# Kernel optimization log

Measured on AMD Instinct MI355X. Metric: run time of the kernel, lower is better.

Reference implementation:

```python
import jax, jax.numpy as jnp
import numpy as np

N, NFEAT, K, HK = 500000, 64, 8, 64

def _trunc_normal(key, shape, std):
    # torch.nn.init.trunc_normal_ truncates at +/-2 (then scaled by std)
    return jnp.clip(jax.random.normal(key, shape), -2.0, 2.0) * std

def setup_inputs() -> dict:
    key = jax.random.key(0)
    kx, kz, kt = jax.random.split(key, 3)
    x = jax.random.normal(kx, (N, NFEAT), dtype=jnp.float32)
    # stacked ParameterList: z[i] in R^{h_K x n}, t[i] in R^{h_K}
    z = _trunc_normal(kz, (K, HK, NFEAT), 1.0).astype(jnp.float32)  # b_z = 1.0
    t = _trunc_normal(kt, (K, HK), 1.0).astype(jnp.float32)         # b_t = 1.0
    return {"x": x, "z": z, "t": t}

def reference(x, z, t):
    w = jnp.exp(z)                                  # [K, HK, n], positive weights
    g = jnp.einsum('ni,khi->nkh', x, w) + t         # [N, K, HK]
    max_vals = jnp.max(g, axis=2)                   # [N, K] maxout per group
    max_idx = jnp.argmax(g, axis=2)                 # [N, K]
    y = jnp.min(max_vals, axis=1)                   # [N]   min over groups
    min_idx = jnp.argmin(max_vals, axis=1)          # [N]
    # A[min_idx[n], max_idx[n, min_idx[n]]] += 1  (vectorized scatter-add)
    cols = jnp.take_along_axis(max_idx, min_idx[:, None], axis=1)[:, 0]  # [N]
    A = jnp.zeros((K, HK), dtype=jnp.float32).at[min_idx, cols].add(1.0)
    return y, A
```

## Files before the change

### kernel.cpp

```cpp
#include <hip/hip_runtime.h>
#include <math.h>

constexpr int NS    = 500000;
constexpr int NF    = 64;
constexpr int KG    = 8;
constexpr int HKC   = 64;
constexpr int NCELL = KG * HKC;
constexpr int RPW   = 32;
constexpr int TPB   = 1024;
constexpr int NBLK  = 256;
constexpr int NTILE = NS / RPW;
constexpr int NWAVES = NBLK * (TPB / 64);

typedef __attribute__((ext_vector_type(8))) _Float16 half8;
typedef __attribute__((ext_vector_type(4))) float f32x4;

__device__ __forceinline__ float swz16_f(float v) {
    return __int_as_float(__builtin_amdgcn_ds_swizzle(__float_as_int(v), 0x401F));
}
__device__ __forceinline__ int swz16_i(int v) {
    return __builtin_amdgcn_ds_swizzle(v, 0x401F);
}

__global__ void prep_kernel(const float* __restrict__ z,
                            _Float16* __restrict__ w_hi,
                            _Float16* __restrict__ w_lo,
                            float* __restrict__ A) {
    int i = blockIdx.x * blockDim.x + threadIdx.x;
    if (i < KG * HKC * NF) {
        float w = expf(z[i]);
        _Float16 h = (_Float16)w;
        w_hi[i] = h;
        w_lo[i] = (_Float16)(w - (float)h);
    }
    if (i < NCELL) A[i] = 0.0f;
}

__global__ __launch_bounds__(TPB, 4) void monn_mfma_kernel(
    const float* __restrict__ x,
    const _Float16* __restrict__ w_hi,
    const _Float16* __restrict__ w_lo,
    const float* __restrict__ t,
    float* __restrict__ y,
    float* __restrict__ A) {

    __shared__ __align__(16) char smem[2 * KG * 8192];
    __shared__ __align__(16) float t_lds[KG * HKC];
    __shared__ unsigned lhist[NCELL];

    const int tid = threadIdx.x;

    {
        const float4* sh = reinterpret_cast<const float4*>(w_hi);
        const float4* sl = reinterpret_cast<const float4*>(w_lo);
#pragma unroll
        for (int i = 0; i < 4; ++i) {
            const int ci  = i * 1024 + tid;
            const int row = (ci >> 3) & 63;
            const int ch  = ci & 7;
            const int addr = (ci >> 9) * 8192 + row * 128 + ((ch ^ (row & 7)) << 4);
            *reinterpret_cast<float4*>(smem + addr)         = sh[ci];
            *reinterpret_cast<float4*>(smem + 65536 + addr) = sl[ci];
        }
        if (tid < 128)
            reinterpret_cast<float4*>(t_lds)[tid] =
                reinterpret_cast<const float4*>(t)[tid];
        if (tid < NCELL) lhist[tid] = 0u;
    }
    __syncthreads();

    const int lane = tid & 63;
    const int m  = lane & 15;
    const int q  = lane >> 4;
    const int q4 = q * 4;
    const int a32 = ((lane ^ 32) << 2);
    const int x7  = m & 7;
    const int rb0 = m * 128 + (((0 + q) ^ x7) << 4);
    const int rb1 = m * 128 + (((4 + q) ^ x7) << 4);
    const int gwave = blockIdx.x * (TPB / 64) + (tid >> 6);

#pragma unroll 1
    for (int tile = gwave; tile < NTILE; tile += NWAVES) {
        const long base = (long)tile * RPW;

        half8 Xh[2][2], Xl[2][2];
#pragma unroll
        for (int rt = 0; rt < 2; ++rt) {
            const float* xp = x + (base + rt * 16 + m) * NF;
#pragma unroll
            for (int s = 0; s < 2; ++s) {
                const int k0 = s * 32 + q * 8;
                const float4 v0 = *reinterpret_cast<const float4*>(xp + k0);
                const float4 v1 = *reinterpret_cast<const float4*>(xp + k0 + 4);
                const float f[8] = {v0.x, v0.y, v0.z, v0.w, v1.x, v1.y, v1.z, v1.w};
#pragma unroll
                for (int j = 0; j < 8; ++j) {
                    _Float16 h = (_Float16)f[j];
                    Xh[rt][s][j] = h;
                    Xl[rt][s][j] = (_Float16)(f[j] - (float)h);
                }
            }
        }

        float ymin[2] = {INFINITY, INFINITY};
        int   code[2] = {0, 0};

#pragma unroll 2
        for (int g = 0; g < KG; ++g) {
            f32x4 acc[4][2];
#pragma unroll
            for (int c = 0; c < 4; ++c) {
                const float4 tv = *reinterpret_cast<const float4*>(
                    t_lds + g * HKC + c * 16 + q4);
                acc[c][0] = (f32x4){tv.x, tv.y, tv.z, tv.w};
                acc[c][1] = acc[c][0];
            }

#pragma unroll
            for (int s = 0; s < 2; ++s) {
                const int rb = (s ? rb1 : rb0) + g * 8192;
#pragma unroll
                for (int c = 0; c < 4; ++c) {
                    const half8 Wh = *reinterpret_cast<const half8*>(
                        smem + rb + c * 2048);
                    const half8 Wl = *reinterpret_cast<const half8*>(
                        smem + 65536 + rb + c * 2048);
                    acc[c][0] = __builtin_amdgcn_mfma_f32_16x16x32_f16(Wh, Xh[0][s], acc[c][0], 0, 0, 0);
                    acc[c][1] = __builtin_amdgcn_mfma_f32_16x16x32_f16(Wh, Xh[1][s], acc[c][1], 0, 0, 0);
                    acc[c][0] = __builtin_amdgcn_mfma_f32_16x16x32_f16(Wl, Xh[0][s], acc[c][0], 0, 0, 0);
                    acc[c][1] = __builtin_amdgcn_mfma_f32_16x16x32_f16(Wl, Xh[1][s], acc[c][1], 0, 0, 0);
                    acc[c][0] = __builtin_amdgcn_mfma_f32_16x16x32_f16(Wh, Xl[0][s], acc[c][0], 0, 0, 0);
                    acc[c][1] = __builtin_amdgcn_mfma_f32_16x16x32_f16(Wh, Xl[1][s], acc[c][1], 0, 0, 0);
                }
            }

#pragma unroll
            for (int rt = 0; rt < 2; ++rt) {
                float t01 = fmaxf(acc[0][rt][0], acc[0][rt][1]);
                float t23 = fmaxf(acc[0][rt][2], acc[0][rt][3]);
                float t45 = fmaxf(acc[1][rt][0], acc[1][rt][1]);
                float t67 = fmaxf(acc[1][rt][2], acc[1][rt][3]);
                float t89 = fmaxf(acc[2][rt][0], acc[2][rt][1]);
                float tab = fmaxf(acc[2][rt][2], acc[2][rt][3]);
                float tcd = fmaxf(acc[3][rt][0], acc[3][rt][1]);
                float tef = fmaxf(acc[3][rt][2], acc[3][rt][3]);
                float v = fmaxf(fmaxf(fmaxf(t01, t23), fmaxf(t45, t67)),
                                fmaxf(fmaxf(t89, tab), fmaxf(tcd, tef)));
                int h = 0;
#pragma unroll
                for (int c = 3; c >= 0; --c)
#pragma unroll
                    for (int j = 3; j >= 0; --j)
                        h = (acc[c][rt][j] == v) ? (c * 16 + j) : h;
                h |= q4;
                {
                    float v2 = swz16_f(v);
                    int   h2 = swz16_i(h);
                    bool take = (v2 > v) || (v2 == v && h2 < h);
                    v = take ? v2 : v;  h = take ? h2 : h;
                    float v3 = __int_as_float(__builtin_amdgcn_ds_bpermute(a32, __float_as_int(v)));
                    int   h3 = __builtin_amdgcn_ds_bpermute(a32, h);
                    take = (v3 > v) || (v3 == v && h3 < h);
                    v = take ? v3 : v;  h = take ? h3 : h;
                }
                const bool better = v < ymin[rt];
                ymin[rt] = fminf(ymin[rt], v);
                code[rt] = better ? ((g << 6) | h) : code[rt];
            }
        }

        if (q == 0) {
#pragma unroll
            for (int rt = 0; rt < 2; ++rt) {
                y[base + rt * 16 + m] = ymin[rt];
                atomicAdd(&lhist[code[rt]], 1u);
            }
        }
    }

    __syncthreads();
    for (int i = tid; i < NCELL; i += TPB) {
        const unsigned c = lhist[i];
        if (c) atomicAdd(&A[i], (float)c);
    }
}

extern "C" void kernel_launch(void* const* d_in, const int* in_sizes, int n_in,
                              void* d_out, int out_size, void* d_ws, size_t ws_size,
                              hipStream_t stream) {
    const float* x = (const float*)d_in[0];
    const float* z = (const float*)d_in[1];
    const float* t = (const float*)d_in[2];

    float* y = (float*)d_out;
    float* A = (float*)d_out + NS;

    _Float16* w_hi = (_Float16*)d_ws;
    _Float16* w_lo = w_hi + (size_t)KG * HKC * NF;

    prep_kernel<<<128, 256, 0, stream>>>(z, w_hi, w_lo, A);
    monn_mfma_kernel<<<NBLK, TPB, 0, stream>>>(x, w_hi, w_lo, t, y, A);
}
```

Before: 234.8 us.

## Double 64-row wave tiles and overlap next group's MFMAs with epilogue

After: 663.7 us. 2.83x slower.

```diff
diff --git a/kernel.cpp b/kernel.cpp
--- a/kernel.cpp
+++ b/kernel.cpp
@@ -6,10 +6,10 @@
 constexpr int KG    = 8;
 constexpr int HKC   = 64;
 constexpr int NCELL = KG * HKC;
-constexpr int RPW   = 32;
-constexpr int TPB   = 1024;
+constexpr int RPW   = 64;
+constexpr int TPB   = 512;
 constexpr int NBLK  = 256;
-constexpr int NTILE = NS / RPW;
+constexpr int NTILE = (NS + RPW - 1) / RPW;
 constexpr int NWAVES = NBLK * (TPB / 64);
 
 typedef __attribute__((ext_vector_type(8))) _Float16 half8;
@@ -36,7 +36,7 @@
     if (i < NCELL) A[i] = 0.0f;
 }
 
-__global__ __launch_bounds__(TPB, 4) void monn_mfma_kernel(
+__global__ __launch_bounds__(TPB, 2) void monn_mfma_kernel(
     const float* __restrict__ x,
     const _Float16* __restrict__ w_hi,
     const _Float16* __restrict__ w_lo,
@@ -54,8 +54,8 @@
         const float4* sh = reinterpret_cast<const float4*>(w_hi);
         const float4* sl = reinterpret_cast<const float4*>(w_lo);
 #pragma unroll
-        for (int i = 0; i < 4; ++i) {
-            const int ci  = i * 1024 + tid;
+        for (int i = 0; i < 8; ++i) {
+            const int ci  = i * 512 + tid;
             const int row = (ci >> 3) & 63;
             const int ch  = ci & 7;
             const int addr = (ci >> 9) * 8192 + row * 128 + ((ch ^ (row & 7)) << 4);
@@ -65,7 +65,7 @@
         if (tid < 128)
             reinterpret_cast<float4*>(t_lds)[tid] =
                 reinterpret_cast<const float4*>(t)[tid];
-        if (tid < NCELL) lhist[tid] = 0u;
+        lhist[tid] = 0u;
     }
     __syncthreads();
 
@@ -83,10 +83,12 @@
     for (int tile = gwave; tile < NTILE; tile += NWAVES) {
         const long base = (long)tile * RPW;
 
-        half8 Xh[2][2], Xl[2][2];
-#pragma unroll
-        for (int rt = 0; rt < 2; ++rt) {
-            const float* xp = x + (base + rt * 16 + m) * NF;
+        half8 Xh[4][2], Xl[4][2];
+#pragma unroll
+        for (int rt = 0; rt < 4; ++rt) {
+            long r = base + rt * 16 + m;
+            r = (r < NS) ? r : (NS - 1);
+            const float* xp = x + r * NF;
 #pragma unroll
             for (int s = 0; s < 2; ++s) {
                 const int k0 = s * 32 + q * 8;
@@ -102,40 +104,44 @@
             }
         }
 
-        float ymin[2] = {INFINITY, INFINITY};
-        int   code[2] = {0, 0};
-
-#pragma unroll 2
-        for (int g = 0; g < KG; ++g) {
-            f32x4 acc[4][2];
+        float ymin[4] = {INFINITY, INFINITY, INFINITY, INFINITY};
+        int   code[4] = {0, 0, 0, 0};
+        f32x4 accA[4][4], accB[4][4];
+
+        auto acc_init = [&](f32x4 (&acc)[4][4], int g) {
 #pragma unroll
             for (int c = 0; c < 4; ++c) {
                 const float4 tv = *reinterpret_cast<const float4*>(
                     t_lds + g * HKC + c * 16 + q4);
-                acc[c][0] = (f32x4){tv.x, tv.y, tv.z, tv.w};
-                acc[c][1] = acc[c][0];
-            }
-
-#pragma unroll
-            for (int s = 0; s < 2; ++s) {
-                const int rb = (s ? rb1 : rb0) + g * 8192;
-#pragma unroll
-                for (int c = 0; c < 4; ++c) {
-                    const half8 Wh = *reinterpret_cast<const half8*>(
-                        smem + rb + c * 2048);
-                    const half8 Wl = *reinterpret_cast<const half8*>(
-                        smem + 65536 + rb + c * 2048);
-                    acc[c][0] = __builtin_amdgcn_mfma_f32_16x16x32_f16(Wh, Xh[0][s], acc[c][0], 0, 0, 0);
-                    acc[c][1] = __builtin_amdgcn_mfma_f32_16x16x32_f16(Wh, Xh[1][s], acc[c][1], 0, 0, 0);
-                    acc[c][0] = __builtin_amdgcn_mfma_f32_16x16x32_f16(Wl, Xh[0][s], acc[c][0], 0, 0, 0);
-                    acc[c][1] = __builtin_amdgcn_mfma_f32_16x16x32_f16(Wl, Xh[1][s], acc[c][1], 0, 0, 0);
-                    acc[c][0] = __builtin_amdgcn_mfma_f32_16x16x32_f16(Wh, Xl[0][s], acc[c][0], 0, 0, 0);
-                    acc[c][1] = __builtin_amdgcn_mfma_f32_16x16x32_f16(Wh, Xl[1][s], acc[c][1], 0, 0, 0);
-                }
-            }
-
-#pragma unroll
-            for (int rt = 0; rt < 2; ++rt) {
+                const f32x4 tin = (f32x4){tv.x, tv.y, tv.z, tv.w};
+#pragma unroll
+                for (int rt = 0; rt < 4; ++rt) acc[c][rt] = tin;
+            }
+        };
+
+        auto mfma_half = [&](f32x4 (&acc)[4][4], int g, int s) {
+            const int rb = (s ? rb1 : rb0) + g * 8192;
+#pragma unroll
+            for (int c = 0; c < 4; ++c) {
+                const half8 Wh = *reinterpret_cast<const half8*>(
+                    smem + rb + c * 2048);
+                const half8 Wl = *reinterpret_cast<const half8*>(
+                    smem + 65536 + rb + c * 2048);
+#pragma unroll
+                for (int rt = 0; rt < 4; ++rt)
+                    acc[c][rt] = __builtin_amdgcn_mfma_f32_16x16x32_f16(Wh, Xh[rt][s], acc[c][rt], 0, 0, 0);
+#pragma unroll
+                for (int rt = 0; rt < 4; ++rt)
+                    acc[c][rt] = __builtin_amdgcn_mfma_f32_16x16x32_f16(Wl, Xh[rt][s], acc[c][rt], 0, 0, 0);
+#pragma unroll
+                for (int rt = 0; rt < 4; ++rt)
+                    acc[c][rt] = __builtin_amdgcn_mfma_f32_16x16x32_f16(Wh, Xl[rt][s], acc[c][rt], 0, 0, 0);
+            }
+        };
+
+        auto epilogue = [&](f32x4 (&acc)[4][4], int g) {
+#pragma unroll
+            for (int rt = 0; rt < 4; ++rt) {
                 float t01 = fmaxf(acc[0][rt][0], acc[0][rt][1]);
                 float t23 = fmaxf(acc[0][rt][2], acc[0][rt][3]);
                 float t45 = fmaxf(acc[1][rt][0], acc[1][rt][1]);
@@ -167,21 +173,43 @@
                 ymin[rt] = fminf(ymin[rt], v);
                 code[rt] = better ? ((g << 6) | h) : code[rt];
             }
-        }
+        };
+
+        acc_init(accA, 0);
+        mfma_half(accA, 0, 0);
+        mfma_half(accA, 0, 1);
+#pragma unroll
+        for (int g = 1; g < KG; ++g) {
+            if (g & 1) {
+                acc_init(accB, g);
+                mfma_half(accB, g, 0);
+                epilogue(accA, g - 1);
+                mfma_half(accB, g, 1);
+            } else {
+                acc_init(accA, g);
+                mfma_half(accA, g, 0);
+                epilogue(accB, g - 1);
+                mfma_half(accA, g, 1);
+            }
+        }
+        epilogue(accB, KG - 1);
 
         if (q == 0) {
 #pragma unroll
-            for (int rt = 0; rt < 2; ++rt) {
-                y[base + rt * 16 + m] = ymin[rt];
-                atomicAdd(&lhist[code[rt]], 1u);
+            for (int rt = 0; rt < 4; ++rt) {
+                const long r = base + rt * 16 + m;
+                if (r < NS) {
+                    y[r] = ymin[rt];
+                    atomicAdd(&lhist[code[rt]], 1u);
+                }
             }
         }
     }
 
     __syncthreads();
-    for (int i = tid; i < NCELL; i += TPB) {
-        const unsigned c = lhist[i];
-        if (c) atomicAdd(&A[i], (float)c);
+    {
+        const unsigned c = lhist[tid];
+        if (c) atomicAdd(&A[tid], (float)c);
     }
 }
 
```

## Switch GEMM to 32x32x16 MFMA with linear pre-permuted LDS weight layout

Applied to the files above, without the earlier changes.

After: 234.4 us. No clear change (-0.2%).

```diff
diff --git a/kernel.cpp b/kernel.cpp
--- a/kernel.cpp
+++ b/kernel.cpp
@@ -12,15 +12,8 @@
 constexpr int NTILE = NS / RPW;
 constexpr int NWAVES = NBLK * (TPB / 64);
 
-typedef __attribute__((ext_vector_type(8))) _Float16 half8;
-typedef __attribute__((ext_vector_type(4))) float f32x4;
-
-__device__ __forceinline__ float swz16_f(float v) {
-    return __int_as_float(__builtin_amdgcn_ds_swizzle(__float_as_int(v), 0x401F));
-}
-__device__ __forceinline__ int swz16_i(int v) {
-    return __builtin_amdgcn_ds_swizzle(v, 0x401F);
-}
+typedef __attribute__((ext_vector_type(8)))  _Float16 half8;
+typedef __attribute__((ext_vector_type(16))) float    f32x16;
 
 __global__ void prep_kernel(const float* __restrict__ z,
                             _Float16* __restrict__ w_hi,
@@ -55,12 +48,14 @@
         const float4* sl = reinterpret_cast<const float4*>(w_lo);
 #pragma unroll
         for (int i = 0; i < 4; ++i) {
-            const int ci  = i * 1024 + tid;
-            const int row = (ci >> 3) & 63;
-            const int ch  = ci & 7;
-            const int addr = (ci >> 9) * 8192 + row * 128 + ((ch ^ (row & 7)) << 4);
-            *reinterpret_cast<float4*>(smem + addr)         = sh[ci];
-            *reinterpret_cast<float4*>(smem + 65536 + addr) = sl[ci];
+            const int ci = i * 1024 + tid;
+            const int l  = ci & 63;
+            const int ks = (ci >> 6) & 3;
+            const int c  = (ci >> 8) & 1;
+            const int g  = ci >> 9;
+            const int gi = (g * 64 + c * 32 + (l & 31)) * 8 + ks * 2 + (l >> 5);
+            *reinterpret_cast<float4*>(smem + ci * 16)         = sh[gi];
+            *reinterpret_cast<float4*>(smem + 65536 + ci * 16) = sl[gi];
         }
         if (tid < 128)
             reinterpret_cast<float4*>(t_lds)[tid] =
@@ -70,111 +65,106 @@
     __syncthreads();
 
     const int lane = tid & 63;
-    const int m  = lane & 15;
-    const int q  = lane >> 4;
-    const int q4 = q * 4;
-    const int a32 = ((lane ^ 32) << 2);
-    const int x7  = m & 7;
-    const int rb0 = m * 128 + (((0 + q) ^ x7) << 4);
-    const int rb1 = m * 128 + (((4 + q) ^ x7) << 4);
+    const int col  = lane & 31;
+    const int hig  = lane >> 5;
+    const int hi4  = hig * 4;
+    const int a32  = ((lane ^ 32) << 2);
+    const int wb   = lane * 16;
     const int gwave = blockIdx.x * (TPB / 64) + (tid >> 6);
 
 #pragma unroll 1
     for (int tile = gwave; tile < NTILE; tile += NWAVES) {
         const long base = (long)tile * RPW;
 
-        half8 Xh[2][2], Xl[2][2];
+        half8 Xh[4], Xl[4];
+        {
+            const float* xp = x + (base + col) * NF + hig * 8;
 #pragma unroll
-        for (int rt = 0; rt < 2; ++rt) {
-            const float* xp = x + (base + rt * 16 + m) * NF;
-#pragma unroll
-            for (int s = 0; s < 2; ++s) {
-                const int k0 = s * 32 + q * 8;
-                const float4 v0 = *reinterpret_cast<const float4*>(xp + k0);
-                const float4 v1 = *reinterpret_cast<const float4*>(xp + k0 + 4);
+            for (int ks = 0; ks < 4; ++ks) {
+                const float4 v0 = *reinterpret_cast<const float4*>(xp + ks * 16);
+                const float4 v1 = *reinterpret_cast<const float4*>(xp + ks * 16 + 4);
                 const float f[8] = {v0.x, v0.y, v0.z, v0.w, v1.x, v1.y, v1.z, v1.w};
 #pragma unroll
                 for (int j = 0; j < 8; ++j) {
                     _Float16 h = (_Float16)f[j];
-                    Xh[rt][s][j] = h;
-                    Xl[rt][s][j] = (_Float16)(f[j] - (float)h);
+                    Xh[ks][j] = h;
+                    Xl[ks][j] = (_Float16)(f[j] - (float)h);
                 }
             }
         }
 
-        float ymin[2] = {INFINITY, INFINITY};
-        int   code[2] = {0, 0};
+        float ymin = INFINITY;
+        int   code = 0;
 
-#pragma unroll 2
+#pragma unroll 1
         for (int g = 0; g < KG; ++g) {
-            f32x4 acc[4][2];
+            f32x16 acc[2];
 #pragma unroll
-            for (int c = 0; c < 4; ++c) {
-                const float4 tv = *reinterpret_cast<const float4*>(
-                    t_lds + g * HKC + c * 16 + q4);
-                acc[c][0] = (f32x4){tv.x, tv.y, tv.z, tv.w};
-                acc[c][1] = acc[c][0];
+            for (int c = 0; c < 2; ++c)
+#pragma unroll
+                for (int Q = 0; Q < 4; ++Q) {
+                    const float4 tv = *reinterpret_cast<const float4*>(
+                        t_lds + g * HKC + c * 32 + 8 * Q + hi4);
+                    acc[c][4 * Q + 0] = tv.x;
+                    acc[c][4 * Q + 1] = tv.y;
+                    acc[c][4 * Q + 2] = tv.z;
+                    acc[c][4 * Q + 3] = tv.w;
+                }
+
+#pragma unroll
+            for (int ks = 0; ks < 4; ++ks) {
+                const int ob = g * 8192 + ks * 1024 + wb;
+                const half8 Wh0 = *reinterpret_cast<const half8*>(smem + ob);
+                const half8 Wh1 = *reinterpret_cast<const half8*>(smem + ob + 4096);
+                const half8 Wl0 = *reinterpret_cast<const half8*>(smem + 65536 + ob);
+                const half8 Wl1 = *reinterpret_cast<const half8*>(smem + 65536 + ob + 4096);
+                acc[0] = __builtin_amdgcn_mfma_f32_32x32x16_f16(Wh0, Xh[ks], acc[0], 0, 0, 0);
+                acc[1] = __builtin_amdgcn_mfma_f32_32x32x16_f16(Wh1, Xh[ks], acc[1], 0, 0, 0);
+                acc[0] = __builtin_amdgcn_mfma_f32_32x32x16_f16(Wl0, Xh[ks], acc[0], 0, 0, 0);
+                acc[1] = __builtin_amdgcn_mfma_f32_32x32x16_f16(Wl1, Xh[ks], acc[1], 0, 0, 0);
+                acc[0] = __builtin_amdgcn_mfma_f32_32x32x16_f16(Wh0, Xl[ks], acc[0], 0, 0, 0);
+                acc[1] = __builtin_amdgcn_mfma_f32_32x32x16_f16(Wh1, Xl[ks], acc[1], 0, 0, 0);
             }
 
+            float qm[2][4];
 #pragma unroll
-            for (int s = 0; s < 2; ++s) {
-                const int rb = (s ? rb1 : rb0) + g * 8192;
+            for (int c = 0; c < 2; ++c)
 #pragma unroll
-                for (int c = 0; c < 4; ++c) {
-                    const half8 Wh = *reinterpret_cast<const half8*>(
-                        smem + rb + c * 2048);
-                    const half8 Wl = *reinterpret_cast<const half8*>(
-                        smem + 65536 + rb + c * 2048);
-                    acc[c][0] = __builtin_amdgcn_mfma_f32_16x16x32_f16(Wh, Xh[0][s], acc[c][0], 0, 0, 0);
-                    acc[c][1] = __builtin_amdgcn_mfma_f32_16x16x32_f16(Wh, Xh[1][s], acc[c][1], 0, 0, 0);
-                    acc[c][0] = __builtin_amdgcn_mfma_f32_16x16x32_f16(Wl, Xh[0][s], acc[c][0], 0, 0, 0);
-                    acc[c][1] = __builtin_amdgcn_mfma_f32_16x16x32_f16(Wl, Xh[1][s], acc[c][1], 0, 0, 0);
-                    acc[c][0] = __builtin_amdgcn_mfma_f32_16x16x32_f16(Wh, Xl[0][s], acc[c][0], 0, 0, 0);
-                    acc[c][1] = __builtin_amdgcn_mfma_f32_16x16x32_f16(Wh, Xl[1][s], acc[c][1], 0, 0, 0);
-                }
-            }
-
+                for (int Q = 0; Q < 4; ++Q)
+                    qm[c][Q] = fmaxf(fmaxf(acc[c][4 * Q], acc[c][4 * Q + 1]),
+                                     fmaxf(acc[c][4 * Q + 2], acc[c][4 * Q + 3]));
+            float v = fmaxf(fmaxf(fmaxf(qm[0][0], qm[0][1]), fmaxf(qm[0][2], qm[0][3])),
+                            fmaxf(fmaxf(qm[1][0], qm[1][1]), fmaxf(qm[1][2], qm[1][3])));
+            int jq[2][4] = {{0, 0, 0, 0}, {0, 0, 0, 0}};
 #pragma unroll
-            for (int rt = 0; rt < 2; ++rt) {
-                float t01 = fmaxf(acc[0][rt][0], acc[0][rt][1]);
-                float t23 = fmaxf(acc[0][rt][2], acc[0][rt][3]);
-                float t45 = fmaxf(acc[1][rt][0], acc[1][rt][1]);
-                float t67 = fmaxf(acc[1][rt][2], acc[1][rt][3]);
-                float t89 = fmaxf(acc[2][rt][0], acc[2][rt][1]);
-                float tab = fmaxf(acc[2][rt][2], acc[2][rt][3]);
-                float tcd = fmaxf(acc[3][rt][0], acc[3][rt][1]);
-                float tef = fmaxf(acc[3][rt][2], acc[3][rt][3]);
-                float v = fmaxf(fmaxf(fmaxf(t01, t23), fmaxf(t45, t67)),
-                                fmaxf(fmaxf(t89, tab), fmaxf(tcd, tef)));
-                int h = 0;
+            for (int c = 0; c < 2; ++c)
 #pragma unroll
-                for (int c = 3; c >= 0; --c)
+                for (int Q = 0; Q < 4; ++Q)
 #pragma unroll
                     for (int j = 3; j >= 0; --j)
-                        h = (acc[c][rt][j] == v) ? (c * 16 + j) : h;
-                h |= q4;
-                {
-                    float v2 = swz16_f(v);
-                    int   h2 = swz16_i(h);
-                    bool take = (v2 > v) || (v2 == v && h2 < h);
-                    v = take ? v2 : v;  h = take ? h2 : h;
-                    float v3 = __int_as_float(__builtin_amdgcn_ds_bpermute(a32, __float_as_int(v)));
-                    int   h3 = __builtin_amdgcn_ds_bpermute(a32, h);
-                    take = (v3 > v) || (v3 == v && h3 < h);
-                    v = take ? v3 : v;  h = take ? h3 : h;
-                }
-                const bool better = v < ymin[rt];
-                ymin[rt] = fminf(ymin[rt], v);
-                code[rt] = better ? ((g << 6) | h) : code[rt];
+                        jq[c][Q] = (acc[c][4 * Q + j] == v) ? j : jq[c][Q];
+            int h = 0;
+#pragma unroll
+            for (int c = 1; c >= 0; --c)
+#pragma unroll
+                for (int Q = 3; Q >= 0; --Q)
+                    h = (qm[c][Q] == v) ? (c * 32 + 8 * Q + jq[c][Q]) : h;
+            h |= hi4;
+            {
+                const float v2 = __int_as_float(
+                    __builtin_amdgcn_ds_bpermute(a32, __float_as_int(v)));
+                const int h2 = __builtin_amdgcn_ds_bpermute(a32, h);
+                const bool take = (v2 > v) || (v2 == v && h2 < h);
+                v = take ? v2 : v;  h = take ? h2 : h;
             }
+            const bool better = v < ymin;
+            ymin = fminf(ymin, v);
+            code = better ? ((g << 6) | h) : code;
         }
 
-        if (q == 0) {
-#pragma unroll
-            for (int rt = 0; rt < 2; ++rt) {
-                y[base + rt * 16 + m] = ymin[rt];
-                atomicAdd(&lhist[code[rt]], 1u);
-            }
+        if (lane < 32) {
+            y[base + col] = ymin;
+            atomicAdd(&lhist[code], 1u);
         }
     }
 
```

## Split groups across block pairs and merge per-row minima via 64-bit atomicMin

Applied to the files above, without the earlier changes.

Result: slower. 248.5 us (+5.8%).

```diff
diff --git a/kernel.cpp b/kernel.cpp
--- a/kernel.cpp
+++ b/kernel.cpp
@@ -6,11 +6,12 @@
 constexpr int KG    = 8;
 constexpr int HKC   = 64;
 constexpr int NCELL = KG * HKC;
-constexpr int RPW   = 32;
+constexpr int SLICE = HKC * NF;
+constexpr int RPT   = 16;
+constexpr int NTILE = NS / RPT;
 constexpr int TPB   = 1024;
-constexpr int NBLK  = 256;
-constexpr int NTILE = NS / RPW;
-constexpr int NWAVES = NBLK * (TPB / 64);
+constexpr int BPH   = (NTILE + 15) / 16;
+constexpr int NBLK  = 2 * BPH;
 
 typedef __attribute__((ext_vector_type(8))) _Float16 half8;
 typedef __attribute__((ext_vector_type(4))) float f32x4;
@@ -20,13 +21,19 @@
 }
 __device__ __forceinline__ int swz16_i(int v) {
     return __builtin_amdgcn_ds_swizzle(v, 0x401F);
+}
+
+__device__ __forceinline__ unsigned fkey(float v) {
+    const unsigned b = __float_as_uint(v);
+    return (b & 0x80000000u) ? ~b : (b | 0x80000000u);
 }
 
 __global__ void prep_kernel(const float* __restrict__ z,
                             _Float16* __restrict__ w_hi,
                             _Float16* __restrict__ w_lo,
-                            float* __restrict__ A) {
-    int i = blockIdx.x * blockDim.x + threadIdx.x;
+                            float* __restrict__ A,
+                            unsigned long long* __restrict__ minkey) {
+    const int i = blockIdx.x * blockDim.x + threadIdx.x;
     if (i < KG * HKC * NF) {
         float w = expf(z[i]);
         _Float16 h = (_Float16)w;
@@ -34,40 +41,44 @@
         w_lo[i] = (_Float16)(w - (float)h);
     }
     if (i < NCELL) A[i] = 0.0f;
-}
-
-__global__ __launch_bounds__(TPB, 4) void monn_mfma_kernel(
+    for (int j = i; j < NS; j += 512 * 256)
+        minkey[j] = 0xFFFFFFFFFFFFFFFFull;
+}
+
+__global__ __launch_bounds__(TPB, 8) void monn_mfma_kernel(
     const float* __restrict__ x,
     const _Float16* __restrict__ w_hi,
     const _Float16* __restrict__ w_lo,
     const float* __restrict__ t,
-    float* __restrict__ y,
-    float* __restrict__ A) {
-
-    __shared__ __align__(16) char smem[2 * KG * 8192];
-    __shared__ __align__(16) float t_lds[KG * HKC];
-    __shared__ unsigned lhist[NCELL];
-
-    const int tid = threadIdx.x;
+    unsigned long long* __restrict__ minkey) {
+
+    __shared__ __align__(16) char smem[2 * 4 * 8192];
+    __shared__ __align__(16) float t_lds[4 * HKC];
+
+    const int tid   = threadIdx.x;
+    const int half  = blockIdx.x & 1;
+    const int gbase = half * 4;
 
     {
-        const float4* sh = reinterpret_cast<const float4*>(w_hi);
-        const float4* sl = reinterpret_cast<const float4*>(w_lo);
-#pragma unroll
-        for (int i = 0; i < 4; ++i) {
+        const float4* sh = reinterpret_cast<const float4*>(w_hi + (size_t)gbase * SLICE);
+        const float4* sl = reinterpret_cast<const float4*>(w_lo + (size_t)gbase * SLICE);
+#pragma unroll
+        for (int i = 0; i < 2; ++i) {
             const int ci  = i * 1024 + tid;
             const int row = (ci >> 3) & 63;
             const int ch  = ci & 7;
             const int addr = (ci >> 9) * 8192 + row * 128 + ((ch ^ (row & 7)) << 4);
             *reinterpret_cast<float4*>(smem + addr)         = sh[ci];
-            *reinterpret_cast<float4*>(smem + 65536 + addr) = sl[ci];
-        }
-        if (tid < 128)
+            *reinterpret_cast<float4*>(smem + 32768 + addr) = sl[ci];
+        }
+        if (tid < 64)
             reinterpret_cast<float4*>(t_lds)[tid] =
-                reinterpret_cast<const float4*>(t)[tid];
-        if (tid < NCELL) lhist[tid] = 0u;
+                reinterpret_cast<const float4*>(t + gbase * HKC)[tid];
     }
     __syncthreads();
+
+    const int tile = (blockIdx.x >> 1) * 16 + (tid >> 6);
+    if (tile >= NTILE) return;
 
     const int lane = tid & 63;
     const int m  = lane & 15;
@@ -77,109 +88,108 @@
     const int x7  = m & 7;
     const int rb0 = m * 128 + (((0 + q) ^ x7) << 4);
     const int rb1 = m * 128 + (((4 + q) ^ x7) << 4);
-    const int gwave = blockIdx.x * (TPB / 64) + (tid >> 6);
+
+    const long base = (long)tile * RPT;
+
+    half8 Xh[2], Xl[2];
+    {
+        const float* xp = x + (base + m) * NF;
+#pragma unroll
+        for (int s = 0; s < 2; ++s) {
+            const int k0 = s * 32 + q * 8;
+            const float4 v0 = *reinterpret_cast<const float4*>(xp + k0);
+            const float4 v1 = *reinterpret_cast<const float4*>(xp + k0 + 4);
+            const float f[8] = {v0.x, v0.y, v0.z, v0.w, v1.x, v1.y, v1.z, v1.w};
+#pragma unroll
+            for (int j = 0; j < 8; ++j) {
+                _Float16 h = (_Float16)f[j];
+                Xh[s][j] = h;
+                Xl[s][j] = (_Float16)(f[j] - (float)h);
+            }
+        }
+    }
+
+    float bestv = INFINITY;
+    int   bestc = 0;
 
 #pragma unroll 1
-    for (int tile = gwave; tile < NTILE; tile += NWAVES) {
-        const long base = (long)tile * RPW;
-
-        half8 Xh[2][2], Xl[2][2];
-#pragma unroll
-        for (int rt = 0; rt < 2; ++rt) {
-            const float* xp = x + (base + rt * 16 + m) * NF;
-#pragma unroll
-            for (int s = 0; s < 2; ++s) {
-                const int k0 = s * 32 + q * 8;
-                const float4 v0 = *reinterpret_cast<const float4*>(xp + k0);
-                const float4 v1 = *reinterpret_cast<const float4*>(xp + k0 + 4);
-                const float f[8] = {v0.x, v0.y, v0.z, v0.w, v1.x, v1.y, v1.z, v1.w};
-#pragma unroll
-                for (int j = 0; j < 8; ++j) {
-                    _Float16 h = (_Float16)f[j];
-                    Xh[rt][s][j] = h;
-                    Xl[rt][s][j] = (_Float16)(f[j] - (float)h);
-                }
+    for (int g = 0; g < 4; ++g) {
+        f32x4 acc[4];
+#pragma unroll
+        for (int c = 0; c < 4; ++c) {
+            const float4 tv = *reinterpret_cast<const float4*>(
+                t_lds + g * HKC + c * 16 + q4);
+            acc[c] = (f32x4){tv.x, tv.y, tv.z, tv.w};
+        }
+
+#pragma unroll
+        for (int s = 0; s < 2; ++s) {
+            const int rb = (s ? rb1 : rb0) + g * 8192;
+#pragma unroll
+            for (int c = 0; c < 4; ++c) {
+                const half8 Wh = *reinterpret_cast<const half8*>(smem + rb + c * 2048);
+                const half8 Wl = *reinterpret_cast<const half8*>(smem + 32768 + rb + c * 2048);
+                acc[c] = __builtin_amdgcn_mfma_f32_16x16x32_f16(Wh, Xh[s], acc[c], 0, 0, 0);
+                acc[c] = __builtin_amdgcn_mfma_f32_16x16x32_f16(Wl, Xh[s], acc[c], 0, 0, 0);
+                acc[c] = __builtin_amdgcn_mfma_f32_16x16x32_f16(Wh, Xl[s], acc[c], 0, 0, 0);
             }
         }
 
-        float ymin[2] = {INFINITY, INFINITY};
-        int   code[2] = {0, 0};
-
-#pragma unroll 2
-        for (int g = 0; g < KG; ++g) {
-            f32x4 acc[4][2];
-#pragma unroll
-            for (int c = 0; c < 4; ++c) {
-                const float4 tv = *reinterpret_cast<const float4*>(
-                    t_lds + g * HKC + c * 16 + q4);
-                acc[c][0] = (f32x4){tv.x, tv.y, tv.z, tv.w};
-                acc[c][1] = acc[c][0];
-            }
-
-#pragma unroll
-            for (int s = 0; s < 2; ++s) {
-                const int rb = (s ? rb1 : rb0) + g * 8192;
-#pragma unroll
-                for (int c = 0; c < 4; ++c) {
-                    const half8 Wh = *reinterpret_cast<const half8*>(
-                        smem + rb + c * 2048);
-                    const half8 Wl = *reinterpret_cast<const half8*>(
-                        smem + 65536 + rb + c * 2048);
-                    acc[c][0] = __builtin_amdgcn_mfma_f32_16x16x32_f16(Wh, Xh[0][s], acc[c][0], 0, 0, 0);
-                    acc[c][1] = __builtin_amdgcn_mfma_f32_16x16x32_f16(Wh, Xh[1][s], acc[c][1], 0, 0, 0);
-                    acc[c][0] = __builtin_amdgcn_mfma_f32_16x16x32_f16(Wl, Xh[0][s], acc[c][0], 0, 0, 0);
-                    acc[c][1] = __builtin_amdgcn_mfma_f32_16x16x32_f16(Wl, Xh[1][s], acc[c][1], 0, 0, 0);
-                    acc[c][0] = __builtin_amdgcn_mfma_f32_16x16x32_f16(Wh, Xl[0][s], acc[c][0], 0, 0, 0);
-                    acc[c][1] = __builtin_amdgcn_mfma_f32_16x16x32_f16(Wh, Xl[1][s], acc[c][1], 0, 0, 0);
-                }
-            }
-
-#pragma unroll
-            for (int rt = 0; rt < 2; ++rt) {
-                float t01 = fmaxf(acc[0][rt][0], acc[0][rt][1]);
-                float t23 = fmaxf(acc[0][rt][2], acc[0][rt][3]);
-                float t45 = fmaxf(acc[1][rt][0], acc[1][rt][1]);
-                float t67 = fmaxf(acc[1][rt][2], acc[1][rt][3]);
-                float t89 = fmaxf(acc[2][rt][0], acc[2][rt][1]);
-                float tab = fmaxf(acc[2][rt][2], acc[2][rt][3]);
-                float tcd = fmaxf(acc[3][rt][0], acc[3][rt][1]);
-                float tef = fmaxf(acc[3][rt][2], acc[3][rt][3]);
-                float v = fmaxf(fmaxf(fmaxf(t01, t23), fmaxf(t45, t67)),
-                                fmaxf(fmaxf(t89, tab), fmaxf(tcd, tef)));
-                int h = 0;
-#pragma unroll
-                for (int c = 3; c >= 0; --c)
-#pragma unroll
-                    for (int j = 3; j >= 0; --j)
-                        h = (acc[c][rt][j] == v) ? (c * 16 + j) : h;
-                h |= q4;
-                {
-                    float v2 = swz16_f(v);
-                    int   h2 = swz16_i(h);
-                    bool take = (v2 > v) || (v2 == v && h2 < h);
-                    v = take ? v2 : v;  h = take ? h2 : h;
-                    float v3 = __int_as_float(__builtin_amdgcn_ds_bpermute(a32, __float_as_int(v)));
-                    int   h3 = __builtin_amdgcn_ds_bpermute(a32, h);
-                    take = (v3 > v) || (v3 == v && h3 < h);
-                    v = take ? v3 : v;  h = take ? h3 : h;
-                }
-                const bool better = v < ymin[rt];
-                ymin[rt] = fminf(ymin[rt], v);
-                code[rt] = better ? ((g << 6) | h) : code[rt];
-            }
-        }
-
-        if (q == 0) {
-#pragma unroll
-            for (int rt = 0; rt < 2; ++rt) {
-                y[base + rt * 16 + m] = ymin[rt];
-                atomicAdd(&lhist[code[rt]], 1u);
-            }
-        }
-    }
-
+        float t01 = fmaxf(acc[0][0], acc[0][1]);
+        float t23 = fmaxf(acc[0][2], acc[0][3]);
+        float t45 = fmaxf(acc[1][0], acc[1][1]);
+        float t67 = fmaxf(acc[1][2], acc[1][3]);
+        float t89 = fmaxf(acc[2][0], acc[2][1]);
+        float tab = fmaxf(acc[2][2], acc[2][3]);
+        float tcd = fmaxf(acc[3][0], acc[3][1]);
+        float tef = fmaxf(acc[3][2], acc[3][3]);
+        float v = fmaxf(fmaxf(fmaxf(t01, t23), fmaxf(t45, t67)),
+                        fmaxf(fmaxf(t89, tab), fmaxf(tcd, tef)));
+        int h = 0;
+#pragma unroll
+        for (int c = 3; c >= 0; --c)
+#pragma unroll
+            for (int j = 3; j >= 0; --j)
+                h = (acc[c][j] == v) ? (c * 16 + j) : h;
+        h |= q4;
+        {
+            float v2 = swz16_f(v);
+            int   h2 = swz16_i(h);
+            bool take = (v2 > v) || (v2 == v && h2 < h);
+            v = take ? v2 : v;  h = take ? h2 : h;
+            float v3 = __int_as_float(__builtin_amdgcn_ds_bpermute(a32, __float_as_int(v)));
+            int   h3 = __builtin_amdgcn_ds_bpermute(a32, h);
+            take = (v3 > v) || (v3 == v && h3 < h);
+            v = take ? v3 : v;  h = take ? h3 : h;
+        }
+        const bool better = v < bestv;
+        bestv = fminf(bestv, v);
+        bestc = better ? (((gbase + g) << 6) | h) : bestc;
+    }
+
+    if (q == 0) {
+        const unsigned long long key =
+            ((unsigned long long)fkey(bestv) << 32) | (unsigned)bestc;
+        atomicMin(&minkey[base + m], key);
+    }
+}
+
+__global__ void final_kernel(const unsigned long long* __restrict__ minkey,
+                             float* __restrict__ y,
+                             float* __restrict__ A) {
+    __shared__ unsigned lhist[NCELL];
+    const int tid = threadIdx.x;
+    for (int i = tid; i < NCELL; i += 256) lhist[i] = 0u;
     __syncthreads();
-    for (int i = tid; i < NCELL; i += TPB) {
+    for (int i = blockIdx.x * 256 + tid; i < NS; i += gridDim.x * 256) {
+        const unsigned long long key = minkey[i];
+        const unsigned k = (unsigned)(key >> 32);
+        const unsigned b = (k & 0x80000000u) ? (k ^ 0x80000000u) : ~k;
+        y[i] = __uint_as_float(b);
+        atomicAdd(&lhist[(unsigned)key & (NCELL - 1)], 1u);
+    }
+    __syncthreads();
+    for (int i = tid; i < NCELL; i += 256) {
         const unsigned c = lhist[i];
         if (c) atomicAdd(&A[i], (float)c);
     }
@@ -197,7 +207,10 @@
 
     _Float16* w_hi = (_Float16*)d_ws;
     _Float16* w_lo = w_hi + (size_t)KG * HKC * NF;
-
-    prep_kernel<<<128, 256, 0, stream>>>(z, w_hi, w_lo, A);
-    monn_mfma_kernel<<<NBLK, TPB, 0, stream>>>(x, w_hi, w_lo, t, y, A);
-}
+    unsigned long long* minkey =
+        (unsigned long long*)((char*)d_ws + 2 * sizeof(_Float16) * KG * HKC * NF);
+
+    prep_kernel<<<512, 256, 0, stream>>>(z, w_hi, w_lo, A, minkey);
+    monn_mfma_kernel<<<NBLK, TPB, 0, stream>>>(x, w_hi, w_lo, t, minkey);
+    final_kernel<<<512, 256, 0, stream>>>(minkey, y, A);
+}
```
